# Optimization experiments

Hardware: AMD Instinct MI355X
Metric: run time of the kernel (lower is better)

## Reference

```python
import jax, jax.numpy as jnp
import numpy as np

D = 1536          # model dim
N = 12            # num heads
HD = D // N       # head dim = 128
C = HD // 2       # rope complex channels = 64
F, H, W = 4, 32, 32
L = F * H * W     # 4096 tokens
B = 1
S1 = C - 2 * (C // 3)   # 22 channels for the frame axis
S2 = C // 3             # 21 channels each for h and w axes
EPS = 1e-6


def setup_inputs() -> dict:
    key = jax.random.key(0)
    ks = jax.random.split(key, 9)
    sc = 1.0 / np.sqrt(D)
    inp = {"x": jax.random.normal(ks[0], (B, L, D), jnp.float32)}
    for i, name in enumerate(["wq", "wk", "wv", "wo"]):
        inp[name] = jax.random.normal(ks[1 + i], (D, D), jnp.float32) * sc
    for i, name in enumerate(["bq", "bk", "bv", "bo"]):
        inp[name] = jax.random.normal(ks[5 + i], (D,), jnp.float32) * 0.01
    inp["gq"] = jnp.ones((D,), jnp.float32)
    inp["gk"] = jnp.ones((D,), jnp.float32)
    # precomputed rotary tables: angle[pos, j] = pos * theta_j (complex freqs = cos + i sin)
    pos = jnp.arange(1024, dtype=jnp.float32)
    inv = 10000.0 ** (-jnp.arange(C, dtype=jnp.float32) / C)
    ang = pos[:, None] * inv[None, :]
    inp["freqs_cos"] = jnp.cos(ang)
    inp["freqs_sin"] = jnp.sin(ang)
    inp["seq_lens"] = jnp.full((B,), L, dtype=jnp.int32)
    inp["f_size"] = F
    inp["h_size"] = H
    inp["w_size"] = W
    return inp


def _rms(y, g):
    return y * jax.lax.rsqrt(jnp.mean(y * y, axis=-1, keepdims=True) + EPS) * g


def _grid(tab, f, h, w):
    # concat per-axis frequency bands: [f,h,w, S1 | S2 | rest] -> [L, 1, C]
    a = jnp.broadcast_to(tab[:f, None, None, :S1], (f, h, w, S1))
    b = jnp.broadcast_to(tab[None, :h, None, S1:S1 + S2], (f, h, w, S2))
    c = jnp.broadcast_to(tab[None, None, :w, S1 + S2:], (f, h, w, C - S1 - S2))
    return jnp.concatenate([a, b, c], axis=-1).reshape(f * h * w, 1, C)


def reference(x, wq, bq, wk, bk, wv, bv, wo, bo, gq, gk,
              freqs_cos, freqs_sin, seq_lens, f_size, h_size, w_size):
    b, l, dim = x.shape
    n = N
    d = dim // n
    c = d // 2
    # QKV projections with QK RMSNorm (norm over full model dim, as in the module)
    q = _rms(x @ wq.T + bq, gq).reshape(b, l, n, d)
    k = _rms(x @ wk.T + bk, gk).reshape(b, l, n, d)
    v = (x @ wv.T + bv).reshape(b, l, n, d)
    # 3D rotary: complex multiply by per-position grid frequencies
    cosg = _grid(freqs_cos, f_size, h_size, w_size)  # [L,1,C]
    sing = _grid(freqs_sin, f_size, h_size, w_size)

    def rope(t):
        tr = t.reshape(b, l, n, c, 2)
        xr, xi = tr[..., 0], tr[..., 1]
        return jnp.stack([xr * cosg - xi * sing, xr * sing + xi * cosg], axis=-1).reshape(b, l, n, d)

    q = rope(q)
    k = rope(k)
    # full (non-windowed) scaled dot-product attention, all k_lens == L
    scores = jnp.einsum('blnd,bmnd->bnlm', q, k) / jnp.sqrt(jnp.float32(d))
    attn = jax.nn.softmax(scores, axis=-1)
    out = jnp.einsum('bnlm,bmnd->blnd', attn, v).reshape(b, l, dim)
    return out @ wo.T + bo
```

## Files before the change

### kernel.cpp

```cpp
#include <hip/hip_runtime.h>
#include <math.h>

#define Dm   1536
#define NHd  12
#define HDm  128
#define Ltok 4096
#define S1c  22
#define S2c  21
#define MFIX 5.0f
#define LOG2E 1.4426950408889634f

typedef __attribute__((ext_vector_type(8))) _Float16 f16x8;
typedef __attribute__((ext_vector_type(4))) float f32x4;

static __device__ __forceinline__ f32x4 MFMA16(f16x8 a, f16x8 b, f32x4 c) {
  return __builtin_amdgcn_mfma_f32_16x16x32_f16(a, b, c, 0, 0, 0);
}

static __device__ __forceinline__ unsigned int pack_f16(float a, float b) {
  union { _Float16 h[2]; unsigned int u; } x;
  x.h[0] = (_Float16)a; x.h[1] = (_Float16)b;
  return x.u;
}

static __device__ __forceinline__ void gload_lds16(const void* g, void* l) {
  __builtin_amdgcn_global_load_lds(
      (const __attribute__((address_space(1))) unsigned int*)g,
      (__attribute__((address_space(3))) unsigned int*)l, 16, 0, 0);
}

__global__ __launch_bounds__(256) void cvt_f16(
    const float* __restrict__ src, unsigned short* __restrict__ dst, int nslots)
{
  int i = blockIdx.x * 256 + threadIdx.x;
  if (i >= nslots) return;
  float4 v = *(const float4*)&src[(size_t)i * 4];
  uint2 p;
  p.x = pack_f16(v.x, v.y);
  p.y = pack_f16(v.z, v.w);
  *(uint2*)&dst[(size_t)i * 4] = p;
}

__global__ __launch_bounds__(256) void cvt_w4_f16(
    const float* __restrict__ w0, const float* __restrict__ w1,
    const float* __restrict__ w2, const float* __restrict__ w3,
    unsigned short* __restrict__ dst)
{
  const int which = blockIdx.y;
  const float* src = (which == 0) ? w0 : (which == 1) ? w1 : (which == 2) ? w2 : w3;
  unsigned short* d = dst + (size_t)which * Dm * Dm;
  int i = blockIdx.x * 256 + threadIdx.x;
  float4 v = *(const float4*)&src[(size_t)i * 4];
  uint2 p;
  p.x = pack_f16(v.x, v.y);
  p.y = pack_f16(v.z, v.w);
  *(uint2*)&d[(size_t)i * 4] = p;
}

__global__ __launch_bounds__(256) void gemm_qkv_f16(
    const unsigned short* __restrict__ Ag, const unsigned short* __restrict__ Wg,
    const float* __restrict__ bq, const float* __restrict__ bk,
    const float* __restrict__ bv,
    float* __restrict__ qb, float* __restrict__ kb,
    unsigned short* __restrict__ vT)
{
  __shared__ __align__(16) unsigned short As[2][128][32], Bs[2][128][32];
  const int tid = threadIdx.x;
  const int w = tid >> 6, lane = tid & 63;
  const int nx = lane & 15, g = lane >> 4;
  const int m0 = blockIdx.y * 128, n0 = blockIdx.x * 128;
  const int wr = w >> 1, wc = w & 1;
  const int which = (n0 >= 2 * Dm) ? 2 : ((n0 >= Dm) ? 1 : 0);
  const int n0loc = n0 - which * Dm;

  const int srow = lane >> 2, scol = (lane & 3) * 8;
  const unsigned short* gp;
  char* lbase0;
  if (w < 2) {
    gp = Ag + (size_t)(m0 + w * 64 + srow) * Dm + scol;
    lbase0 = (char*)&As[0][0][0] + w * 4096;
  } else {
    gp = Wg + (size_t)(n0 + (w - 2) * 64 + srow) * Dm + scol;
    lbase0 = (char*)&Bs[0][0][0] + (w - 2) * 4096;
  }

  f32x4 acc[4][4];
#pragma unroll
  for (int i = 0; i < 4; i++)
#pragma unroll
    for (int j = 0; j < 4; j++) acc[i][j] = (f32x4){0.f, 0.f, 0.f, 0.f};

#pragma unroll
  for (int c = 0; c < 4; ++c)
    gload_lds16(gp + (size_t)c * 16 * Dm, lbase0 + c * 1024);
  gp += 32;

  const int NK = Dm / 32;
  for (int it = 0; it < NK; ++it) {
    const int cur = it & 1;
    if (it + 1 < NK) {
      char* lb = lbase0 + (cur ^ 1) * 8192;
#pragma unroll
      for (int c = 0; c < 4; ++c)
        gload_lds16(gp + (size_t)c * 16 * Dm, lb + c * 1024);
      gp += 32;
      asm volatile("s_waitcnt vmcnt(4)" ::: "memory");
    } else {
      asm volatile("s_waitcnt vmcnt(0)" ::: "memory");
    }
    __builtin_amdgcn_s_barrier();
    f16x8 ah[4], bh[4];
#pragma unroll
    for (int i = 0; i < 4; ++i) {
      ah[i] = *(const f16x8*)&As[cur][wr * 64 + i * 16 + nx][g * 8];
      bh[i] = *(const f16x8*)&Bs[cur][wc * 64 + i * 16 + nx][g * 8];
    }
#pragma unroll
    for (int i = 0; i < 4; ++i)
#pragma unroll
      for (int j = 0; j < 4; ++j)
        acc[i][j] = MFMA16(ah[i], bh[j], acc[i][j]);
    __builtin_amdgcn_s_barrier();
  }

  if (which < 2) {
    float* Cout = which ? kb : qb;
    const float* bias = which ? bk : bq;
#pragma unroll
    for (int j = 0; j < 4; ++j) {
      const int col = n0loc + wc * 64 + j * 16 + nx;
      const float bz = bias[col];
#pragma unroll
      for (int i = 0; i < 4; ++i) {
        const int row0 = m0 + wr * 64 + i * 16 + g * 4;
#pragma unroll
        for (int r = 0; r < 4; ++r)
          Cout[(size_t)(row0 + r) * Dm + col] = acc[i][j][r] + bz;
      }
    }
  } else {
#pragma unroll
    for (int j = 0; j < 4; ++j) {
      const int col = n0loc + wc * 64 + j * 16 + nx;
      const float bz = bv[col];
#pragma unroll
      for (int i = 0; i < 4; ++i) {
        const int row0 = m0 + wr * 64 + i * 16 + g * 4;
        uint2 pk;
        pk.x = pack_f16(acc[i][j][0] + bz, acc[i][j][1] + bz);
        pk.y = pack_f16(acc[i][j][2] + bz, acc[i][j][3] + bz);
        *(uint2*)&vT[(size_t)col * Ltok + row0] = pk;
      }
    }
  }
}

__global__ __launch_bounds__(256) void gemm_nt_f16(
    const unsigned short* __restrict__ Ag, const unsigned short* __restrict__ Wg,
    const float* __restrict__ bias, float* __restrict__ Cout)
{
  __shared__ __align__(16) unsigned short As[2][128][32], Bs[2][128][32];
  const int tid = threadIdx.x;
  const int w = tid >> 6, lane = tid & 63;
  const int nx = lane & 15, g = lane >> 4;
  const int m0 = blockIdx.y * 128, n0 = blockIdx.x * 128;
  const int wr = w >> 1, wc = w & 1;

  const int srow = lane >> 2, scol = (lane & 3) * 8;
  const unsigned short* gp;
  char* lbase0;
  if (w < 2) {
    gp = Ag + (size_t)(m0 + w * 64 + srow) * Dm + scol;
    lbase0 = (char*)&As[0][0][0] + w * 4096;
  } else {
    gp = Wg + (size_t)(n0 + (w - 2) * 64 + srow) * Dm + scol;
    lbase0 = (char*)&Bs[0][0][0] + (w - 2) * 4096;
  }

  f32x4 acc[4][4];
#pragma unroll
  for (int i = 0; i < 4; i++)
#pragma unroll
    for (int j = 0; j < 4; j++) acc[i][j] = (f32x4){0.f, 0.f, 0.f, 0.f};

#pragma unroll
  for (int c = 0; c < 4; ++c)
    gload_lds16(gp + (size_t)c * 16 * Dm, lbase0 + c * 1024);
  gp += 32;

  const int NK = Dm / 32;
  for (int it = 0; it < NK; ++it) {
    const int cur = it & 1;
    if (it + 1 < NK) {
      char* lb = lbase0 + (cur ^ 1) * 8192;
#pragma unroll
      for (int c = 0; c < 4; ++c)
        gload_lds16(gp + (size_t)c * 16 * Dm, lb + c * 1024);
      gp += 32;
      asm volatile("s_waitcnt vmcnt(4)" ::: "memory");
    } else {
      asm volatile("s_waitcnt vmcnt(0)" ::: "memory");
    }
    __builtin_amdgcn_s_barrier();
    f16x8 ah[4], bh[4];
#pragma unroll
    for (int i = 0; i < 4; ++i) {
      ah[i] = *(const f16x8*)&As[cur][wr * 64 + i * 16 + nx][g * 8];
      bh[i] = *(const f16x8*)&Bs[cur][wc * 64 + i * 16 + nx][g * 8];
    }
#pragma unroll
    for (int i = 0; i < 4; ++i)
#pragma unroll
      for (int j = 0; j < 4; ++j)
        acc[i][j] = MFMA16(ah[i], bh[j], acc[i][j]);
    __builtin_amdgcn_s_barrier();
  }
#pragma unroll
  for (int j = 0; j < 4; ++j) {
    const int col = n0 + wc * 64 + j * 16 + nx;
    const float bz = bias[col];
#pragma unroll
    for (int i = 0; i < 4; ++i) {
      const int row0 = m0 + wr * 64 + i * 16 + g * 4;
#pragma unroll
      for (int r = 0; r < 4; ++r)
        Cout[(size_t)(row0 + r) * Dm + col] = acc[i][j][r] + bz;
    }
  }
}

__global__ __launch_bounds__(256) void rmsnorm_rope_f16(
    float* __restrict__ q, float* __restrict__ k,
    const float* __restrict__ gq, const float* __restrict__ gk,
    const float* __restrict__ fcos, const float* __restrict__ fsin)
{
  const int l = blockIdx.x;
  const int tid = threadIdx.x;
  const int d0 = tid * 6;
  float qv[6], kv[6];
  float sq = 0.f, sk = 0.f;
  const float* qp = &q[(size_t)l * Dm + d0];
  const float* kp = &k[(size_t)l * Dm + d0];
#pragma unroll
  for (int i = 0; i < 6; i++) {
    qv[i] = qp[i]; sq += qv[i] * qv[i];
    kv[i] = kp[i]; sk += kv[i] * kv[i];
  }
#pragma unroll
  for (int s = 1; s < 64; s <<= 1) {
    sq += __shfl_xor(sq, s);
    sk += __shfl_xor(sk, s);
  }
  __shared__ float redq[4], redk[4];
  if ((tid & 63) == 0) { redq[tid >> 6] = sq; redk[tid >> 6] = sk; }
  __syncthreads();
  sq = redq[0] + redq[1] + redq[2] + redq[3];
  sk = redk[0] + redk[1] + redk[2] + redk[3];
  const float rq = rsqrtf(sq * (1.f / (float)Dm) + 1e-6f);
  const float rk = rsqrtf(sk * (1.f / (float)Dm) + 1e-6f);
  const float qscale = 0.08838834764831845f * LOG2E;
  const int f = l >> 10, h = (l >> 5) & 31, w = l & 31;
  unsigned short* qo = (unsigned short*)q + (size_t)l * Dm;
  unsigned short* ko = (unsigned short*)k + (size_t)l * Dm;
#pragma unroll
  for (int i = 0; i < 3; i++) {
    const int d = d0 + 2 * i;
    const int cc = (d & (HDm - 1)) >> 1;
    const int pos = (cc < S1c) ? f : ((cc < S1c + S2c) ? h : w);
    const float co = fcos[pos * 64 + cc];
    const float si = fsin[pos * 64 + cc];
    const float xr = qv[2 * i]     * rq * gq[d];
    const float xi = qv[2 * i + 1] * rq * gq[d + 1];
    *(unsigned int*)&qo[d] =
        pack_f16((xr * co - xi * si) * qscale, (xr * si + xi * co) * qscale);
    const float yr = kv[2 * i]     * rk * gk[d];
    const float yi = kv[2 * i + 1] * rk * gk[d + 1];
    *(unsigned int*)&ko[d] = pack_f16(yr * co - yi * si, yr * si + yi * co);
  }
}

__global__ __launch_bounds__(256, 3) void attn_f16(
    const unsigned short* __restrict__ qs, const unsigned short* __restrict__ ks,
    const unsigned short* __restrict__ vT,
    float* __restrict__ Op0, float* __restrict__ Op1,
    float* __restrict__ stats)
{
  __shared__ __align__(16) unsigned short Ks[2][32][136];
  __shared__ __align__(16) unsigned short Vs[2][128][40];

  const int tid = threadIdx.x;
  const int w = tid >> 6, lane = tid & 63;
  const int nx = lane & 15, g = lane >> 4;

  const int F = blockIdx.x;
  const int g8 = F & 7;
  const int qb = (F >> 3) & 31;
  const int gdiv = F >> 8;
  const int grp = gdiv * 8 + g8;
  const int head = grp >> 1;
  const int half = grp & 1;

  const int qbase = qb * 128 + w * 32;
  const int kvbase = half * (Ltok / 2);
  float* __restrict__ Op = half ? Op1 : Op0;

  const float NEGMFIX2 = -MFIX * LOG2E;

  f16x8 vones;
#pragma unroll
  for (int i = 0; i < 8; i++) vones[i] = (_Float16)1.0f;

  f16x8 qf[2][4];
#pragma unroll
  for (int s = 0; s < 2; s++) {
    const unsigned short* qp =
        &qs[(size_t)(qbase + s * 16 + nx) * Dm + head * HDm + g * 8];
#pragma unroll
    for (int c = 0; c < 4; c++) qf[s][c] = *(const f16x8*)(qp + c * 32);
  }

  f32x4 oacc[2][9];
#pragma unroll
  for (int s = 0; s < 2; s++)
#pragma unroll
    for (int nt = 0; nt < 9; nt++) oacc[s][nt] = (f32x4){0.f, 0.f, 0.f, 0.f};

  const int krow = tid >> 3, kchb = (tid & 7) << 4;
  const int vrow = tid >> 1, vseg = (tid & 1) << 4;
  const int vofs = (tid & 1) << 2;

  const unsigned short* kg = &ks[(size_t)(kvbase + krow) * Dm + head * HDm + kchb];
  const unsigned short* vg = &vT[((size_t)head * HDm + vrow) * Ltok + kvbase + vseg];

#define VSTORE_PI(buf, va_, vb_)                                              \
  {                                                                           \
    *(uint2*)&Vs[buf][vrow][vofs]      = make_uint2((va_).x, (va_).y);        \
    *(uint2*)&Vs[buf][vrow][8 + vofs]  = make_uint2((va_).z, (va_).w);        \
    *(uint2*)&Vs[buf][vrow][16 + vofs] = make_uint2((vb_).x, (vb_).y);        \
    *(uint2*)&Vs[buf][vrow][24 + vofs] = make_uint2((vb_).z, (vb_).w);        \
  }

  {
    uint4 ka = *(const uint4*)kg, kb4 = *(const uint4*)(kg + 8);
    uint4 va = *(const uint4*)vg, vb4 = *(const uint4*)(vg + 8);
    *(uint4*)&Ks[0][krow][kchb]     = ka;
    *(uint4*)&Ks[0][krow][kchb + 8] = kb4;
    VSTORE_PI(0, va, vb4);
  }
  __syncthreads();

  const int NIT = Ltok / 2 / 32;
  for (int t = 0; t < NIT; t++) {
    const int cur = t & 1, nxt = cur ^ 1;
    const bool pref = (t + 1 < NIT);
    uint4 ka, kb4, va, vb4;
    if (pref) {
      kg += 32 * Dm;
      vg += 32;
      ka  = *(const uint4*)kg;  kb4 = *(const uint4*)(kg + 8);
      va  = *(const uint4*)vg;  vb4 = *(const uint4*)(vg + 8);
    }

    f32x4 sa[2][2];
#pragma unroll
    for (int s = 0; s < 2; s++)
#pragma unroll
      for (int mt = 0; mt < 2; mt++)
        sa[s][mt] = (f32x4){NEGMFIX2, NEGMFIX2, NEGMFIX2, NEGMFIX2};
    __builtin_amdgcn_s_setprio(1);
#pragma unroll
    for (int c = 0; c < 4; c++) {
      f16x8 k0f = *(const f16x8*)&Ks[cur][nx][c * 32 + g * 8];
      f16x8 k1f = *(const f16x8*)&Ks[cur][16 + nx][c * 32 + g * 8];
#pragma unroll
      for (int s = 0; s < 2; s++) {
        sa[s][0] = MFMA16(k0f, qf[s][c], sa[s][0]);
        sa[s][1] = MFMA16(k1f, qf[s][c], sa[s][1]);
      }
    }
    __builtin_amdgcn_s_setprio(0);

    union { unsigned int u[4]; f16x8 v; } ph[2];
#pragma unroll
    for (int s = 0; s < 2; s++) {
      float p[8];
#pragma unroll
      for (int r = 0; r < 4; r++) {
        p[r]     = __builtin_amdgcn_exp2f(sa[s][0][r]);
        p[4 + r] = __builtin_amdgcn_exp2f(sa[s][1][r]);
      }
      ph[s].u[0] = pack_f16(p[0], p[1]);
      ph[s].u[1] = pack_f16(p[2], p[3]);
      ph[s].u[2] = pack_f16(p[4], p[5]);
      ph[s].u[3] = pack_f16(p[6], p[7]);
    }

    __builtin_amdgcn_s_setprio(1);
#pragma unroll
    for (int nt = 0; nt < 8; nt++) {
      f16x8 vh = *(const f16x8*)&Vs[cur][nt * 16 + nx][g * 8];
#pragma unroll
      for (int s = 0; s < 2; s++)
        oacc[s][nt] = MFMA16(ph[s].v, vh, oacc[s][nt]);
    }
#pragma unroll
    for (int s = 0; s < 2; s++)
      oacc[s][8] = MFMA16(ph[s].v, vones, oacc[s][8]);
    __builtin_amdgcn_s_setprio(0);

    if (pref) {
      *(uint4*)&Ks[nxt][krow][kchb]     = ka;
      *(uint4*)&Ks[nxt][krow][kchb + 8] = kb4;
      VSTORE_PI(nxt, va, vb4);
    }
    __syncthreads();
  }
#undef VSTORE_PI

#pragma unroll
  for (int s = 0; s < 2; s++) {
#pragma unroll
    for (int nt = 0; nt < 8; nt++)
#pragma unroll
      for (int r = 0; r < 4; r++)
        Op[(size_t)(qbase + s * 16 + g * 4 + r) * Dm + head * HDm + nt * 16 + nx] =
            oacc[s][nt][r];
    if (nx == 0) {
#pragma unroll
      for (int r = 0; r < 4; r++)
        stats[((size_t)half * Ltok + qbase + s * 16 + g * 4 + r) * NHd + head] =
            oacc[s][8][r];
    }
  }
}

__global__ __launch_bounds__(384) void combine_f16(
    const float* __restrict__ Op0, const float* __restrict__ Op1,
    const float* __restrict__ stats, unsigned short* __restrict__ oh)
{
  const int row = blockIdx.x;
  const int c4 = threadIdx.x * 4;
  const int head = c4 >> 7;
  const float l0 = stats[(size_t)row * NHd + head];
  const float l1 = stats[((size_t)Ltok + row) * NHd + head];
  const float rl = 1.f / (l0 + l1);
  float4 o0 = *(const float4*)&Op0[(size_t)row * Dm + c4];
  float4 o1 = *(const float4*)&Op1[(size_t)row * Dm + c4];
  uint2 p;
  p.x = pack_f16((o0.x + o1.x) * rl, (o0.y + o1.y) * rl);
  p.y = pack_f16((o0.z + o1.z) * rl, (o0.w + o1.w) * rl);
  *(uint2*)&oh[(size_t)row * Dm + c4] = p;
}

extern "C" void kernel_launch(void* const* d_in, const int* in_sizes, int n_in,
                              void* d_out, int out_size, void* d_ws, size_t ws_size,
                              hipStream_t stream)
{
  const float* x    = (const float*)d_in[0];
  const float* wq   = (const float*)d_in[1];
  const float* wk   = (const float*)d_in[2];
  const float* wv   = (const float*)d_in[3];
  const float* wo   = (const float*)d_in[4];
  const float* bq   = (const float*)d_in[5];
  const float* bk   = (const float*)d_in[6];
  const float* bv   = (const float*)d_in[7];
  const float* bo   = (const float*)d_in[8];
  const float* gq   = (const float*)d_in[9];
  const float* gk   = (const float*)d_in[10];
  const float* fcos = (const float*)d_in[11];
  const float* fsin = (const float*)d_in[12];
  float* out = (float*)d_out;

  const size_t LD = (size_t)Ltok * Dm;
  const size_t WH = (size_t)Dm * Dm;
  float* base = (float*)d_ws;
  float* qb = base;
  float* kb = base + LD;
  unsigned short* vT  = (unsigned short*)(base + 2 * LD);
  unsigned short* xh  = (unsigned short*)(base + 2 * LD + LD / 2);
  float* Op0 = base + 2 * LD + LD / 2;
  float* Op1 = Op0 + LD;
  unsigned short* wqh = (unsigned short*)(Op1 + LD);
  unsigned short* woh = wqh + 3 * WH;
  unsigned short* oh  = (unsigned short*)base;
  float* stats = (float*)(wqh + 4 * WH);

  const int xslots = (int)(LD / 4);
  const int w4     = (int)(WH / 4);
  dim3 gqkv(3 * Dm / 128, Ltok / 128);
  dim3 gout(Dm / 128, Ltok / 128);

  cvt_f16<<<(xslots + 255) / 256, 256, 0, stream>>>(x, xh, xslots);
  cvt_w4_f16<<<dim3(w4 / 256, 4), 256, 0, stream>>>(wq, wk, wv, wo, wqh);

  gemm_qkv_f16<<<gqkv, 256, 0, stream>>>(xh, wqh, bq, bk, bv, qb, kb, vT);
  rmsnorm_rope_f16<<<Ltok, 256, 0, stream>>>(qb, kb, gq, gk, fcos, fsin);
  attn_f16<<<dim3(768, 1, 1), 256, 0, stream>>>(
      (const unsigned short*)qb, (const unsigned short*)kb, vT, Op0, Op1, stats);
  combine_f16<<<Ltok, 384, 0, stream>>>(Op0, Op1, stats, oh);
  gemm_nt_f16<<<gout, 256, 0, stream>>>(oh, woh, bo, out);
}
```

Before: 399.9 us.

## Load K fragments directly from global into registers and sum row denominators in VALU

The attention kernel no longer stages K tiles through shared memory. Each lane loads its K MFMA fragments straight from global memory into registers, prefetched one iteration ahead. The softmax denominator is now summed in VALU with cross-lane shuffles instead of an extra MFMA against a ones vector. This removes the LDS writes and reads for K and two MFMAs per iteration. In exchange every wave of the block reloads the same K data from global or cache, and register pressure goes up from the eight prefetched K vectors.

```diff
diff --git a/kernel.cpp b/kernel.cpp
--- a/kernel.cpp
+++ b/kernel.cpp
@@ -285,7 +285,6 @@
     float* __restrict__ Op0, float* __restrict__ Op1,
     float* __restrict__ stats)
 {
-  __shared__ __align__(16) unsigned short Ks[2][32][136];
   __shared__ __align__(16) unsigned short Vs[2][128][40];
 
   const int tid = threadIdx.x;
@@ -306,10 +305,6 @@
 
   const float NEGMFIX2 = -MFIX * LOG2E;
 
-  f16x8 vones;
-#pragma unroll
-  for (int i = 0; i < 8; i++) vones[i] = (_Float16)1.0f;
-
   f16x8 qf[2][4];
 #pragma unroll
   for (int s = 0; s < 2; s++) {
@@ -319,18 +314,32 @@
     for (int c = 0; c < 4; c++) qf[s][c] = *(const f16x8*)(qp + c * 32);
   }
 
-  f32x4 oacc[2][9];
+  f32x4 oacc[2][8];
 #pragma unroll
   for (int s = 0; s < 2; s++)
 #pragma unroll
-    for (int nt = 0; nt < 9; nt++) oacc[s][nt] = (f32x4){0.f, 0.f, 0.f, 0.f};
-
-  const int krow = tid >> 3, kchb = (tid & 7) << 4;
+    for (int nt = 0; nt < 8; nt++) oacc[s][nt] = (f32x4){0.f, 0.f, 0.f, 0.f};
+  float lrow[2] = {0.f, 0.f};
+
   const int vrow = tid >> 1, vseg = (tid & 1) << 4;
   const int vofs = (tid & 1) << 2;
 
-  const unsigned short* kg = &ks[(size_t)(kvbase + krow) * Dm + head * HDm + kchb];
   const unsigned short* vg = &vT[((size_t)head * HDm + vrow) * Ltok + kvbase + vseg];
+
+  const unsigned short* kp0 = &ks[(size_t)(kvbase + nx) * Dm + head * HDm + g * 8];
+  f16x8 kf[8];
+#define KLOAD(T)                                                              \
+  {                                                                           \
+    const unsigned short* kp_ = kp0 + (size_t)(T) * 32 * Dm;                  \
+    kf[0] = *(const f16x8*)(kp_);                                             \
+    kf[1] = *(const f16x8*)(kp_ + 32);                                        \
+    kf[2] = *(const f16x8*)(kp_ + 64);                                        \
+    kf[3] = *(const f16x8*)(kp_ + 96);                                        \
+    kf[4] = *(const f16x8*)(kp_ + 16 * Dm);                                   \
+    kf[5] = *(const f16x8*)(kp_ + 16 * Dm + 32);                              \
+    kf[6] = *(const f16x8*)(kp_ + 16 * Dm + 64);                              \
+    kf[7] = *(const f16x8*)(kp_ + 16 * Dm + 96);                              \
+  }
 
 #define VSTORE_PI(buf, va_, vb_)                                              \
   {                                                                           \
@@ -340,11 +349,9 @@
     *(uint2*)&Vs[buf][vrow][24 + vofs] = make_uint2((vb_).z, (vb_).w);        \
   }
 
+  KLOAD(0);
   {
-    uint4 ka = *(const uint4*)kg, kb4 = *(const uint4*)(kg + 8);
     uint4 va = *(const uint4*)vg, vb4 = *(const uint4*)(vg + 8);
-    *(uint4*)&Ks[0][krow][kchb]     = ka;
-    *(uint4*)&Ks[0][krow][kchb + 8] = kb4;
     VSTORE_PI(0, va, vb4);
   }
   __syncthreads();
@@ -353,13 +360,6 @@
   for (int t = 0; t < NIT; t++) {
     const int cur = t & 1, nxt = cur ^ 1;
     const bool pref = (t + 1 < NIT);
-    uint4 ka, kb4, va, vb4;
-    if (pref) {
-      kg += 32 * Dm;
-      vg += 32;
-      ka  = *(const uint4*)kg;  kb4 = *(const uint4*)(kg + 8);
-      va  = *(const uint4*)vg;  vb4 = *(const uint4*)(vg + 8);
-    }
 
     f32x4 sa[2][2];
 #pragma unroll
@@ -370,25 +370,33 @@
     __builtin_amdgcn_s_setprio(1);
 #pragma unroll
     for (int c = 0; c < 4; c++) {
-      f16x8 k0f = *(const f16x8*)&Ks[cur][nx][c * 32 + g * 8];
-      f16x8 k1f = *(const f16x8*)&Ks[cur][16 + nx][c * 32 + g * 8];
 #pragma unroll
       for (int s = 0; s < 2; s++) {
-        sa[s][0] = MFMA16(k0f, qf[s][c], sa[s][0]);
-        sa[s][1] = MFMA16(k1f, qf[s][c], sa[s][1]);
+        sa[s][0] = MFMA16(kf[c],     qf[s][c], sa[s][0]);
+        sa[s][1] = MFMA16(kf[4 + c], qf[s][c], sa[s][1]);
       }
     }
     __builtin_amdgcn_s_setprio(0);
 
+    uint4 va, vb4;
+    if (pref) {
+      KLOAD(t + 1);
+      vg += 32;
+      va  = *(const uint4*)vg;  vb4 = *(const uint4*)(vg + 8);
+    }
+
     union { unsigned int u[4]; f16x8 v; } ph[2];
 #pragma unroll
     for (int s = 0; s < 2; s++) {
-      float p[8];
+      float p[8], ps = 0.f;
 #pragma unroll
       for (int r = 0; r < 4; r++) {
         p[r]     = __builtin_amdgcn_exp2f(sa[s][0][r]);
         p[4 + r] = __builtin_amdgcn_exp2f(sa[s][1][r]);
       }
+#pragma unroll
+      for (int j = 0; j < 8; j++) ps += p[j];
+      lrow[s] += ps;
       ph[s].u[0] = pack_f16(p[0], p[1]);
       ph[s].u[1] = pack_f16(p[2], p[3]);
       ph[s].u[2] = pack_f16(p[4], p[5]);
@@ -403,34 +411,26 @@
       for (int s = 0; s < 2; s++)
         oacc[s][nt] = MFMA16(ph[s].v, vh, oacc[s][nt]);
     }
-#pragma unroll
-    for (int s = 0; s < 2; s++)
-      oacc[s][8] = MFMA16(ph[s].v, vones, oacc[s][8]);
     __builtin_amdgcn_s_setprio(0);
 
-    if (pref) {
-      *(uint4*)&Ks[nxt][krow][kchb]     = ka;
-      *(uint4*)&Ks[nxt][krow][kchb + 8] = kb4;
-      VSTORE_PI(nxt, va, vb4);
-    }
+    if (pref) VSTORE_PI(nxt, va, vb4);
     __syncthreads();
   }
 #undef VSTORE_PI
+#undef KLOAD
 
 #pragma unroll
   for (int s = 0; s < 2; s++) {
+    lrow[s] += __shfl_xor(lrow[s], 16);
+    lrow[s] += __shfl_xor(lrow[s], 32);
 #pragma unroll
     for (int nt = 0; nt < 8; nt++)
 #pragma unroll
       for (int r = 0; r < 4; r++)
         Op[(size_t)(qbase + s * 16 + g * 4 + r) * Dm + head * HDm + nt * 16 + nx] =
             oacc[s][nt][r];
-    if (nx == 0) {
-#pragma unroll
-      for (int r = 0; r < 4; r++)
-        stats[((size_t)half * Ltok + qbase + s * 16 + g * 4 + r) * NHd + head] =
-            oacc[s][8][r];
-    }
+    if (g == 0)
+      stats[((size_t)half * Ltok + qbase + s * 16 + nx) * NHd + head] = lrow[s];
   }
 }
 
```

Result: slower. 524.6 us (+31.2%).
